# Kernel optimization log

Measured on AMD Instinct MI355X. Metric: run time of the kernel, lower is better.

## Reference

```python
import jax, jax.numpy as jnp
import numpy as np

N = 50000      # nodes
E = 800000     # edges (before self loops)
F_IN = 512     # input feature dim (num_features)
D = 128        # hidden_dim
NBLK = 3       # num_layers - 1
EPS = 1e-5


def _layernorm(x, g, b):
    mu = x.mean(-1, keepdims=True)
    var = ((x - mu) ** 2).mean(-1, keepdims=True)
    return (x - mu) / jnp.sqrt(var + EPS) * g + b


def _gatv2(x, Wl, bl, Wr, br, att, bias, src, dst, n):
    # PyG GATv2Conv, heads=1, eval mode (attention dropout off), self loops in src/dst
    xl = x @ Wl + bl                      # [N, D] messages (x_j side)
    xr = x @ Wr + br                      # [N, D] target side (x_i)
    e = jax.nn.leaky_relu(xl[src] + xr[dst], negative_slope=0.2)  # [E', D]
    score = e @ att                       # [E']
    smax = jax.ops.segment_max(score, dst, num_segments=n)
    ex = jnp.exp(score - smax[dst])
    denom = jax.ops.segment_sum(ex, dst, num_segments=n)
    alpha = ex / denom[dst]               # segment softmax over incoming edges
    out = jax.ops.segment_sum(alpha[:, None] * xl[src], dst, num_segments=n)
    return out + bias


def setup_inputs() -> dict:
    key = jax.random.key(0)
    ks = jax.random.split(key, 32)
    w = lambda k, shape: (jax.random.normal(k, shape, jnp.float32) * 0.02)
    p = {}
    p["x"] = jax.random.normal(ks[0], (N, F_IN), jnp.float32)
    p["edge_index"] = jax.random.randint(ks[1], (2, E), 0, N)
    p["emb_W"] = w(ks[2], (F_IN, D)); p["emb_b"] = jnp.zeros((D,), jnp.float32)
    p["ln1_g"] = jnp.ones((NBLK, D), jnp.float32); p["ln1_b"] = jnp.zeros((NBLK, D), jnp.float32)
    p["gat_Wl"] = w(ks[3], (NBLK, D, D)); p["gat_bl"] = jnp.zeros((NBLK, D), jnp.float32)
    p["gat_Wr"] = w(ks[4], (NBLK, D, D)); p["gat_br"] = jnp.zeros((NBLK, D), jnp.float32)
    p["gat_att"] = w(ks[5], (NBLK, D)); p["gat_bias"] = jnp.zeros((NBLK, D), jnp.float32)
    for i in range(NBLK):
        h = D * (i + 1)  # mlp_ratio = level = i+1
        p[f"mlp_w1_{i}"] = w(ks[6 + 2 * i], (D, h))
        p[f"mlp_w2_{i}"] = w(ks[7 + 2 * i], (h, D))
    p["attn_Wa"] = w(ks[12], (D, D)); p["attn_ba"] = jnp.zeros((D,), jnp.float32)
    p["attn_Wb"] = w(ks[13], (D, D)); p["attn_bb"] = jnp.zeros((D,), jnp.float32)
    p["attn_Wc"] = w(ks[14], (D, 1)); p["attn_bc"] = jnp.zeros((1,), jnp.float32)
    p["rho_W"] = w(ks[15], (D, D)); p["rho_b"] = jnp.zeros((D,), jnp.float32)
    p["cls_W"] = w(ks[16], (D, 4)); p["cls_b"] = jnp.zeros((4,), jnp.float32)
    return p


def reference(x, edge_index, emb_W, emb_b, ln1_g, ln1_b, gat_Wl, gat_bl, gat_Wr, gat_br,
              gat_att, gat_bias, mlp_w1_0, mlp_w2_0, mlp_w1_1, mlp_w2_1, mlp_w1_2, mlp_w2_2,
              attn_Wa, attn_ba, attn_Wb, attn_bb, attn_Wc, attn_bc, rho_W, rho_b, cls_W, cls_b):
    n = x.shape[0]
    sl = jnp.arange(n, dtype=edge_index.dtype)
    src = jnp.concatenate([edge_index[0], sl])  # add self loops (GATv2Conv default)
    dst = jnp.concatenate([edge_index[1], sl])
    h = jax.nn.relu(x @ emb_W + emb_b)          # embedding (dropout off)
    mlps = [(mlp_w1_0, mlp_w2_0), (mlp_w1_1, mlp_w2_1), (mlp_w1_2, mlp_w2_2)]
    for i in range(NBLK):
        hn = _layernorm(h, ln1_g[i], ln1_b[i])
        h = h + _gatv2(hn, gat_Wl[i], gat_bl[i], gat_Wr[i], gat_br[i], gat_att[i], gat_bias[i], src, dst, n)
        w1, w2 = mlps[i]
        # NOTE: original forward applies channel_mix directly on x (norm2 is unused)
        h = h + jax.nn.gelu(h @ w1, approximate=False) @ w2
    # Attn_Net_Gated pooling
    a = jnp.tanh(h @ attn_Wa + attn_ba)
    b = jax.nn.sigmoid(h @ attn_Wb + attn_bb)
    A = ((a * b) @ attn_Wc + attn_bc).T          # [1, N]
    h_path = jax.nn.softmax(A, axis=1) @ h       # [1, D]
    hr = jax.nn.relu(h_path @ rho_W + rho_b)
    logits = hr @ cls_W + cls_b                  # [1, 4]
    Y_hat = jnp.argmax(logits, axis=1, keepdims=True)
    hazards = jax.nn.sigmoid(logits)
    S = jnp.cumprod(1.0 - hazards, axis=1)
    return (hazards, S, Y_hat, logits)
```

## Files before the change

kernel.cpp:

```cpp
#include <hip/hip_runtime.h>
#include <math.h>


#define D 128
#define NBLK 3

typedef __attribute__((ext_vector_type(8))) short bf16x8;
typedef __attribute__((ext_vector_type(4))) float f32x4;

static __device__ __forceinline__ float bf2f(unsigned short u) {
    union { unsigned i; float f; } c; c.i = ((unsigned)u) << 16; return c.f;
}
static __device__ __forceinline__ unsigned short f2bf(float f) {
    union { float f; unsigned i; } c; c.f = f;
    unsigned r = c.i + 0x7fff + ((c.i >> 16) & 1);
    return (unsigned short)(r >> 16);
}

static __device__ __forceinline__ void gl16(const unsigned short* g, unsigned short* l) {
    __builtin_amdgcn_global_load_lds((const __attribute__((address_space(1))) void*)g,
                                     (__attribute__((address_space(3))) void*)l, 16, 0, 0);
}

__global__ void zero_k(int* deg, int* fill, float* red, int n) {
    int i = blockIdx.x * blockDim.x + threadIdx.x;
    if (i < n) { deg[i] = 0; fill[i] = 0; }
    if (i < 132) red[i] = 0.f;
}

__global__ void hist_k(const int* __restrict__ dst, int* __restrict__ deg, int E) {
    int e = blockIdx.x * blockDim.x + threadIdx.x;
    if (e < E) atomicAdd(&deg[dst[e]], 1);
}

__global__ __launch_bounds__(256) void blockscan_k(const int* __restrict__ deg,
                                                   int* __restrict__ rowptr,
                                                   int* __restrict__ bsum, int n) {
    __shared__ int tmp[256];
    const int tid = threadIdx.x;
    const int i = blockIdx.x * 256 + tid;
    int v = (i < n) ? deg[i] : 0;
    tmp[tid] = v;
    __syncthreads();
#pragma unroll
    for (int off = 1; off < 256; off <<= 1) {
        int t = (tid >= off) ? tmp[tid - off] : 0;
        __syncthreads();
        tmp[tid] += t;
        __syncthreads();
    }
    if (i < n) rowptr[i + 1] = tmp[tid];
    if (tid == 255) bsum[blockIdx.x] = tmp[255];
}

__global__ __launch_bounds__(256) void scansums_k(int* __restrict__ bsum, int nb) {
    __shared__ int tmp[256];
    const int tid = threadIdx.x;
    int v = (tid < nb) ? bsum[tid] : 0;
    tmp[tid] = v;
    __syncthreads();
#pragma unroll
    for (int off = 1; off < 256; off <<= 1) {
        int t = (tid >= off) ? tmp[tid - off] : 0;
        __syncthreads();
        tmp[tid] += t;
        __syncthreads();
    }
    if (tid < nb) bsum[tid] = tmp[tid];
}

__global__ __launch_bounds__(256) void addoff_k(int* __restrict__ rowptr,
                                                const int* __restrict__ bsum, int n) {
    int i = blockIdx.x * 256 + threadIdx.x;
    if (i == 0) rowptr[0] = 0;
    if (i < n && blockIdx.x > 0) rowptr[i + 1] += bsum[blockIdx.x - 1];
}

__global__ void scatter_k(const int* __restrict__ src, const int* __restrict__ dst,
                          const int* __restrict__ rowptr, int* __restrict__ fill,
                          int* __restrict__ esrc, int E) {
    int e = blockIdx.x * blockDim.x + threadIdx.x;
    if (e < E) {
        int d = dst[e];
        int pos = rowptr[d] + atomicAdd(&fill[d], 1);
        esrc[pos] = src[e];
    }
}

struct WDesc { const float* s; unsigned short* d; int K; int M; };
struct WPack { WDesc w[21]; };

__global__ __launch_bounds__(256) void wprep_k(WPack p) {
    WDesc d = p.w[blockIdx.y];
    const int nc = d.K / 32;
    const int chunks = (d.M / 16) * nc * 64;
    for (int i = blockIdx.x * 256 + threadIdx.x; i < chunks; i += gridDim.x * 256) {
        const int l = i & 63;
        const int c = (i >> 6) % nc;
        const int t = i / (64 * nc);
        const int m = t * 16 + (l & 15);
        const int kb = c * 32 + ((l >> 4) & 3) * 8;
#pragma unroll
        for (int j = 0; j < 8; ++j)
            d.d[(size_t)i * 8 + j] = f2bf(d.s[(size_t)(kb + j) * d.M + m]);
    }
}

__global__ __launch_bounds__(256) void bcat_k(const float* bl, const float* br,
                                              const float* ba, const float* bb,
                                              float* sb) {
    const int t = threadIdx.x;
    for (int i = 0; i < 3; ++i)
        sb[i * 256 + t] = (t < 128) ? bl[i * 128 + t] : br[i * 128 + t - 128];
    sb[3 * 256 + t] = (t < 128) ? ba[t] : bb[t - 128];
}

template <int NR, bool KM, int ACT, bool BIAS, bool ACC, bool LNM, bool A16,
          bool W32, bool W16>
__global__ __launch_bounds__(256) void rgemm_k(const void* __restrict__ Ap,
                                               const unsigned short* __restrict__ BTc,
                                               const float* __restrict__ bias,
                                               const float* __restrict__ lng,
                                               const float* __restrict__ lnb,
                                               float* __restrict__ C32,
                                               unsigned short* __restrict__ C16,
                                               int N, int strideA, int M) {
    __shared__ unsigned short Bls[128 * 128];
    const int tid = threadIdx.x;
    const int w = tid >> 6, l = tid & 63;
    const int q = l >> 4;
    int r = blockIdx.x * 64 + w * 16 + (l & 15);
    if (r > N - 1) r = N - 1;

    bf16x8 afr[4];
    auto loadA = [&](int koff) {
        if (A16) {
            const unsigned short* A = (const unsigned short*)Ap;
#pragma unroll
            for (int c = 0; c < 4; ++c)
                afr[c] = *(const bf16x8*)(A + (size_t)r * strideA + koff + c * 32 + q * 8);
        } else {
            const float* A = (const float*)Ap;
            float av[4][8];
#pragma unroll
            for (int c = 0; c < 4; ++c) {
                const float* ap = A + (size_t)r * strideA + koff + c * 32 + q * 8;
                const float4 v0 = *(const float4*)ap;
                const float4 v1 = *(const float4*)(ap + 4);
                av[c][0] = v0.x; av[c][1] = v0.y; av[c][2] = v0.z; av[c][3] = v0.w;
                av[c][4] = v1.x; av[c][5] = v1.y; av[c][6] = v1.z; av[c][7] = v1.w;
            }
            if (LNM) {
                float s = 0.f;
#pragma unroll
                for (int c = 0; c < 4; ++c)
#pragma unroll
                    for (int j = 0; j < 8; ++j) s += av[c][j];
                s += __shfl_xor(s, 16, 64); s += __shfl_xor(s, 32, 64);
                const float mu = s * (1.f / 128.f);
                float vv = 0.f;
#pragma unroll
                for (int c = 0; c < 4; ++c)
#pragma unroll
                    for (int j = 0; j < 8; ++j) { const float dd = av[c][j] - mu; vv += dd * dd; }
                vv += __shfl_xor(vv, 16, 64); vv += __shfl_xor(vv, 32, 64);
                const float rs = rsqrtf(vv * (1.f / 128.f) + 1e-5f);
#pragma unroll
                for (int c = 0; c < 4; ++c) {
                    const int kb = c * 32 + q * 8;
                    const float4 g0 = *(const float4*)(lng + kb);
                    const float4 g1 = *(const float4*)(lng + kb + 4);
                    const float4 b0 = *(const float4*)(lnb + kb);
                    const float4 b1 = *(const float4*)(lnb + kb + 4);
                    const float gg[8] = {g0.x, g0.y, g0.z, g0.w, g1.x, g1.y, g1.z, g1.w};
                    const float bb[8] = {b0.x, b0.y, b0.z, b0.w, b1.x, b1.y, b1.z, b1.w};
#pragma unroll
                    for (int j = 0; j < 8; ++j)
                        av[c][j] = (av[c][j] - mu) * rs * gg[j] + bb[j];
                }
            }
#pragma unroll
            for (int c = 0; c < 4; ++c)
#pragma unroll
                for (int j = 0; j < 8; ++j) afr[c][j] = (short)f2bf(av[c][j]);
        }
    };

    f32x4 acc[8];
#pragma unroll
    for (int t = 0; t < 8; ++t) acc[t] = (f32x4){0.f, 0.f, 0.f, 0.f};

    if (!KM) loadA(0);

    const int rb = blockIdx.x * 64 + w * 16 + q * 4;
    auto epi = [&](int col0) {
#pragma unroll
        for (int t = 0; t < 8; ++t) {
            const int col = col0 + t * 16 + (l & 15);
            const float bv = BIAS ? bias[col] : 0.f;
#pragma unroll
            for (int rr = 0; rr < 4; ++rr) {
                const int row = rb + rr;
                if (row >= N) continue;
                float xv = acc[t][rr] + bv;
                if (ACC) xv += C32[(size_t)row * M + col];
                if (ACT == 1) xv = fmaxf(xv, 0.f);
                else if (ACT == 2) xv = 0.5f * xv * (1.f + erff(xv * 0.70710678118654752f));
                if (W32) C32[(size_t)row * M + col] = xv;
                if (W16) C16[(size_t)row * M + col] = f2bf(xv);
            }
        }
    };

#pragma unroll
    for (int rnd = 0; rnd < NR; ++rnd) {
        if (rnd) __syncthreads();
        const unsigned short* bsrc = BTc + (size_t)rnd * 16384;
#pragma unroll
        for (int i = 0; i < 8; ++i) {
            const int idx = i * 256 + tid;
            gl16(bsrc + (size_t)idx * 8, &Bls[idx * 8]);
        }
        if (KM) loadA(rnd * 128);
        __syncthreads();
#pragma unroll
        for (int c = 0; c < 4; ++c)
#pragma unroll
            for (int t = 0; t < 8; ++t) {
                const bf16x8 bfr = *(const bf16x8*)&Bls[((t * 4 + c) * 64 + l) * 8];
                acc[t] = __builtin_amdgcn_mfma_f32_16x16x32_bf16(afr[c], bfr, acc[t], 0, 0, 0);
            }
        if (!KM) {
            epi(rnd * 128);
#pragma unroll
            for (int t = 0; t < 8; ++t) acc[t] = (f32x4){0.f, 0.f, 0.f, 0.f};
        }
    }
    if (KM) epi(0);
}

__global__ __launch_bounds__(256) void gat3_k(const unsigned short* __restrict__ X,
                                              const float* __restrict__ att,
                                              const float* __restrict__ gbias,
                                              const int* __restrict__ rowptr,
                                              const int* __restrict__ esrc,
                                              float* __restrict__ H, int n) {
    const int l = threadIdx.x & 63;
    const int node = blockIdx.x * 4 + (threadIdx.x >> 6);
    if (node >= n) return;
    const int q = l >> 4;
    const int d0 = (l & 15) * 8;

    float a8[8], xr[8], xs[8];
    {
        const float4 t0 = *(const float4*)&att[d0];
        const float4 t1 = *(const float4*)&att[d0 + 4];
        a8[0] = t0.x; a8[1] = t0.y; a8[2] = t0.z; a8[3] = t0.w;
        a8[4] = t1.x; a8[5] = t1.y; a8[6] = t1.z; a8[7] = t1.w;
        const bf16x8 uxs = *(const bf16x8*)&X[(size_t)node * 256 + d0];
        const bf16x8 uxr = *(const bf16x8*)&X[(size_t)node * 256 + 128 + d0];
#pragma unroll
        for (int j = 0; j < 8; ++j) {
            xs[j] = bf2f((unsigned short)uxs[j]);
            xr[j] = bf2f((unsigned short)uxr[j]);
        }
    }

    float sc = 0.f;
#pragma unroll
    for (int j = 0; j < 8; ++j) {
        const float e = xs[j] + xr[j];
        sc = fmaf(a8[j], fmaxf(e, 0.2f * e), sc);
    }
#pragma unroll
    for (int m = 1; m < 16; m <<= 1) sc += __shfl_xor(sc, m, 64);
    const float wself = __expf(sc);
    float dsum = (q == 0) ? wself : 0.f;
    float acc[8];
#pragma unroll
    for (int j = 0; j < 8; ++j) acc[j] = (q == 0) ? wself * xs[j] : 0.f;

    const int p1 = rowptr[node + 1];
    int p = rowptr[node] + q;
    bool v0 = p < p1, v1 = p + 4 < p1, v2 = p + 8 < p1;
    int i2 = v2 ? esrc[p + 8] : 0;
    bf16x8 u0, u1;
    if (v0) u0 = *(const bf16x8*)&X[(size_t)esrc[p] * 256 + d0];
    if (v1) u1 = *(const bf16x8*)&X[(size_t)esrc[p + 4] * 256 + d0];
    while (v0) {
        bf16x8 u2;
        if (v2) u2 = *(const bf16x8*)&X[(size_t)i2 * 256 + d0];
        const bool v3 = p + 12 < p1;
        const int i3 = v3 ? esrc[p + 12] : 0;

        float xl[8];
#pragma unroll
        for (int j = 0; j < 8; ++j) xl[j] = bf2f((unsigned short)u0[j]);
        float e_sc = 0.f;
#pragma unroll
        for (int j = 0; j < 8; ++j) {
            const float e = xl[j] + xr[j];
            e_sc = fmaf(a8[j], fmaxf(e, 0.2f * e), e_sc);
        }
#pragma unroll
        for (int m = 1; m < 16; m <<= 1) e_sc += __shfl_xor(e_sc, m, 64);
        const float wgt = __expf(e_sc);
        dsum += wgt;
#pragma unroll
        for (int j = 0; j < 8; ++j) acc[j] = fmaf(wgt, xl[j], acc[j]);

        u0 = u1; u1 = u2; i2 = i3;
        v0 = v1; v1 = v2; v2 = v3;
        p += 4;
    }

#pragma unroll
    for (int m = 16; m < 64; m <<= 1) {
        dsum += __shfl_xor(dsum, m, 64);
#pragma unroll
        for (int j = 0; j < 8; ++j) acc[j] += __shfl_xor(acc[j], m, 64);
    }

    if (q == 0) {
        const float inv = 1.f / dsum;
        const size_t o = (size_t)node * D + d0;
        float4 h0 = *(const float4*)&H[o];
        float4 h1 = *(const float4*)&H[o + 4];
        float hv[8] = {h0.x, h0.y, h0.z, h0.w, h1.x, h1.y, h1.z, h1.w};
#pragma unroll
        for (int j = 0; j < 8; ++j) hv[j] += acc[j] * inv + gbias[d0 + j];
        *(float4*)&H[o]     = make_float4(hv[0], hv[1], hv[2], hv[3]);
        *(float4*)&H[o + 4] = make_float4(hv[4], hv[5], hv[6], hv[7]);
    }
}

__global__ __launch_bounds__(256) void attnpool_k(const float* __restrict__ H,
                                                  const unsigned short* __restrict__ BTc,
                                                  const float* __restrict__ bias,
                                                  const float* __restrict__ Wc,
                                                  const float* __restrict__ bc,
                                                  float* __restrict__ red, int N) {
    __shared__ unsigned short Bls[128 * 128];
    __shared__ float sacc[4][128];
    __shared__ float sdn[4];
    const int tid = threadIdx.x;
    const int w = tid >> 6, l = tid & 63;
    const int q = l >> 4, l15 = l & 15;
    const int rowbase = blockIdx.x * 64 + w * 16;
    int r = rowbase + l15;
    if (r > N - 1) r = N - 1;

    float av[4][8];
    bf16x8 afr[4];
#pragma unroll
    for (int c = 0; c < 4; ++c) {
        const float* ap = H + (size_t)r * D + c * 32 + q * 8;
        const float4 v0 = *(const float4*)ap;
        const float4 v1 = *(const float4*)(ap + 4);
        av[c][0] = v0.x; av[c][1] = v0.y; av[c][2] = v0.z; av[c][3] = v0.w;
        av[c][4] = v1.x; av[c][5] = v1.y; av[c][6] = v1.z; av[c][7] = v1.w;
#pragma unroll
        for (int j = 0; j < 8; ++j) afr[c][j] = (short)f2bf(av[c][j]);
    }

    float th[8][4];
    f32x4 acc[8];

#pragma unroll
    for (int rnd = 0; rnd < 2; ++rnd) {
        if (rnd) __syncthreads();
        const unsigned short* bsrc = BTc + (size_t)rnd * 16384;
#pragma unroll
        for (int i = 0; i < 8; ++i) {
            const int idx = i * 256 + tid;
            gl16(bsrc + (size_t)idx * 8, &Bls[idx * 8]);
        }
#pragma unroll
        for (int t = 0; t < 8; ++t) acc[t] = (f32x4){0.f, 0.f, 0.f, 0.f};
        __syncthreads();
#pragma unroll
        for (int c = 0; c < 4; ++c)
#pragma unroll
            for (int t = 0; t < 8; ++t) {
                const bf16x8 bfr = *(const bf16x8*)&Bls[((t * 4 + c) * 64 + l) * 8];
                acc[t] = __builtin_amdgcn_mfma_f32_16x16x32_bf16(afr[c], bfr, acc[t], 0, 0, 0);
            }
        if (rnd == 0) {
#pragma unroll
            for (int t = 0; t < 8; ++t) {
                const float bv = bias[t * 16 + l15];
#pragma unroll
                for (int rr = 0; rr < 4; ++rr) th[t][rr] = tanhf(acc[t][rr] + bv);
            }
        }
    }

    float pa[4] = {0.f, 0.f, 0.f, 0.f};
#pragma unroll
    for (int t = 0; t < 8; ++t) {
        const float bv = bias[128 + t * 16 + l15];
        const float wcv = Wc[t * 16 + l15];
#pragma unroll
        for (int rr = 0; rr < 4; ++rr) {
            const float sg = 1.f / (1.f + __expf(-(acc[t][rr] + bv)));
            pa[rr] = fmaf(th[t][rr] * sg, wcv, pa[rr]);
        }
    }
#pragma unroll
    for (int m = 1; m < 16; m <<= 1)
#pragma unroll
        for (int rr = 0; rr < 4; ++rr) pa[rr] += __shfl_xor(pa[rr], m, 64);

    const float bcv = bc[0];
    float wgt[4];
#pragma unroll
    for (int rr = 0; rr < 4; ++rr) {
        const int row = blockIdx.x * 64 + w * 16 + q * 4 + rr;
        wgt[rr] = (row < N) ? __expf(pa[rr] + bcv) : 0.f;
    }
    float s = wgt[0] + wgt[1] + wgt[2] + wgt[3];
    s += __shfl_xor(s, 16, 64);
    s += __shfl_xor(s, 32, 64);
    if (l == 0) sdn[w] = s;

    const int sl = ((l15 >> 2) << 4);
    float wv[4];
#pragma unroll
    for (int rr = 0; rr < 4; ++rr) wv[rr] = __shfl(wgt[rr], sl, 64);
    const int rsel = l15 & 3;
    float wm = (rsel == 0) ? wv[0] : (rsel == 1) ? wv[1] : (rsel == 2) ? wv[2] : wv[3];

#pragma unroll
    for (int c = 0; c < 4; ++c) {
        float pv[8];
#pragma unroll
        for (int j = 0; j < 8; ++j) pv[j] = wm * av[c][j];
#pragma unroll
        for (int m = 1; m < 16; m <<= 1)
#pragma unroll
            for (int j = 0; j < 8; ++j) pv[j] += __shfl_xor(pv[j], m, 64);
        if (l15 == 0) {
#pragma unroll
            for (int j = 0; j < 8; ++j) sacc[w][c * 32 + q * 8 + j] = pv[j];
        }
    }
    __syncthreads();
    if (tid < 128) {
        const float tot = sacc[0][tid] + sacc[1][tid] + sacc[2][tid] + sacc[3][tid];
        atomicAdd(&red[tid], tot);
    }
    if (tid == 0)
        atomicAdd(&red[128], sdn[0] + sdn[1] + sdn[2] + sdn[3]);
}

__global__ __launch_bounds__(128) void final_k(const float* __restrict__ red,
                                               const float* __restrict__ rho_W,
                                               const float* __restrict__ rho_b,
                                               const float* __restrict__ cls_W,
                                               const float* __restrict__ cls_b,
                                               float* __restrict__ out) {
    __shared__ float hp[128];
    __shared__ float hr[128];
    __shared__ float lg[4];
    const int t = threadIdx.x;
    hp[t] = red[t] / red[128];
    __syncthreads();
    float s = rho_b[t];
    for (int k = 0; k < 128; ++k) s = fmaf(hp[k], rho_W[k * 128 + t], s);
    hr[t] = fmaxf(s, 0.f);
    __syncthreads();
    if (t < 4) {
        float l = cls_b[t];
        for (int k = 0; k < 128; ++k) l = fmaf(hr[k], cls_W[k * 4 + t], l);
        lg[t] = l;
    }
    __syncthreads();
    if (t == 0) {
        float hz[4], S[4];
        for (int c = 0; c < 4; ++c) hz[c] = 1.f / (1.f + expf(-lg[c]));
        S[0] = 1.f - hz[0];
        for (int c = 1; c < 4; ++c) S[c] = S[c - 1] * (1.f - hz[c]);
        int am = 0; float bm = lg[0];
        for (int c = 1; c < 4; ++c) if (lg[c] > bm) { bm = lg[c]; am = c; }
        out[0] = hz[0]; out[1] = hz[1]; out[2] = hz[2]; out[3] = hz[3];
        out[4] = S[0];  out[5] = S[1];  out[6] = S[2];  out[7] = S[3];
        out[8] = (float)am;
        out[9] = lg[0]; out[10] = lg[1]; out[11] = lg[2]; out[12] = lg[3];
    }
}

static inline int cdiv(int a, int b) { return (a + b - 1) / b; }

extern "C" void kernel_launch(void* const* d_in, const int* in_sizes, int n_in,
                              void* d_out, int out_size, void* d_ws, size_t ws_size,
                              hipStream_t stream) {
    const float* x      = (const float*)d_in[0];
    const int*   ei     = (const int*)d_in[1];
    const float* emb_W  = (const float*)d_in[2];
    const float* emb_b  = (const float*)d_in[3];
    const float* ln1_g  = (const float*)d_in[4];
    const float* ln1_b  = (const float*)d_in[5];
    const float* gat_Wl = (const float*)d_in[6];
    const float* gat_bl = (const float*)d_in[7];
    const float* gat_Wr = (const float*)d_in[8];
    const float* gat_br = (const float*)d_in[9];
    const float* gat_att  = (const float*)d_in[10];
    const float* gat_bias = (const float*)d_in[11];
    const float* mlp_w1[NBLK] = {(const float*)d_in[12], (const float*)d_in[14], (const float*)d_in[16]};
    const float* mlp_w2[NBLK] = {(const float*)d_in[13], (const float*)d_in[15], (const float*)d_in[17]};
    const float* attn_Wa = (const float*)d_in[18];
    const float* attn_ba = (const float*)d_in[19];
    const float* attn_Wb = (const float*)d_in[20];
    const float* attn_bb = (const float*)d_in[21];
    const float* attn_Wc = (const float*)d_in[22];
    const float* attn_bc = (const float*)d_in[23];
    const float* rho_W   = (const float*)d_in[24];
    const float* rho_b   = (const float*)d_in[25];
    const float* cls_W   = (const float*)d_in[26];
    const float* cls_b   = (const float*)d_in[27];
    float* out = (float*)d_out;

    const int N = in_sizes[0] / 512;
    const int E = in_sizes[1] / 2;
    const int* src = ei;
    const int* dst = ei + E;
    const int gx = cdiv(N, 64);

    char* base = (char*)d_ws;
    float* H = (float*)base;
    unsigned short* X = (unsigned short*)(H + (size_t)N * D);
    unsigned short* T = X + (size_t)N * 256;
    float* red  = (float*)(T + (size_t)N * 384);
    float* sb   = red + 132;
    unsigned short* wbuf = (unsigned short*)(sb + 1024);
    int* esrc   = (int*)(wbuf + 393216);
    int* deg    = esrc + E;
    int* rowptr = deg + N;
    int* fill   = rowptr + N + 1;
    int* bsum   = fill + N;

    unsigned short* embT = wbuf;
    unsigned short* gatT = wbuf + 4 * 16384;
    unsigned short* w1T0 = gatT + 6 * 16384;
    unsigned short* w1T1 = w1T0 + 16384;
    unsigned short* w1T2 = w1T1 + 2 * 16384;
    unsigned short* w2T0 = w1T2 + 3 * 16384;
    unsigned short* w2T1 = w2T0 + 16384;
    unsigned short* w2T2 = w2T1 + 2 * 16384;
    unsigned short* attT = w2T2 + 3 * 16384;
    unsigned short* w1T[NBLK] = {w1T0, w1T1, w1T2};
    unsigned short* w2T[NBLK] = {w2T0, w2T1, w2T2};

    const int nb = cdiv(N, 256);
    zero_k<<<cdiv(N, 256), 256, 0, stream>>>(deg, fill, red, N);
    hist_k<<<cdiv(E, 256), 256, 0, stream>>>(dst, deg, E);
    blockscan_k<<<nb, 256, 0, stream>>>(deg, rowptr, bsum, N);
    scansums_k<<<1, 256, 0, stream>>>(bsum, nb);
    addoff_k<<<nb, 256, 0, stream>>>(rowptr, bsum, N);
    scatter_k<<<cdiv(E, 256), 256, 0, stream>>>(src, dst, rowptr, fill, esrc, E);

    {
        WPack p;
        int di = 0;
        for (int r = 0; r < 4; ++r)
            p.w[di++] = {emb_W + (size_t)r * 128 * 128, embT + (size_t)r * 16384, 128, 128};
        for (int i = 0; i < 3; ++i) {
            p.w[di++] = {gat_Wl + (size_t)i * 16384, gatT + (size_t)(2 * i) * 16384, 128, 128};
            p.w[di++] = {gat_Wr + (size_t)i * 16384, gatT + (size_t)(2 * i + 1) * 16384, 128, 128};
        }
        for (int i = 0; i < 3; ++i)
            p.w[di++] = {mlp_w1[i], w1T[i], 128, 128 * (i + 1)};
        for (int i = 0; i < 3; ++i)
            for (int r = 0; r <= i; ++r)
                p.w[di++] = {mlp_w2[i] + (size_t)r * 128 * 128, w2T[i] + (size_t)r * 16384, 128, 128};
        p.w[di++] = {attn_Wa, attT, 128, 128};
        p.w[di++] = {attn_Wb, attT + 16384, 128, 128};
        wprep_k<<<dim3(32, 21), 256, 0, stream>>>(p);
    }
    bcat_k<<<1, 256, 0, stream>>>(gat_bl, gat_br, attn_ba, attn_bb, sb);

    rgemm_k<4, true, 1, true, false, false, false, true, false>
        <<<gx, 256, 0, stream>>>(x, embT, emb_b, nullptr, nullptr,
                                 H, nullptr, N, 512, 128);

    for (int i = 0; i < NBLK; ++i) {
        rgemm_k<2, false, 0, true, false, true, false, false, true>
            <<<gx, 256, 0, stream>>>(H, gatT + (size_t)(2 * i) * 16384, sb + i * 256,
                                     ln1_g + i * D, ln1_b + i * D, nullptr, X, N, 128, 256);
        gat3_k<<<cdiv(N, 4), 256, 0, stream>>>(X, gat_att + i * D, gat_bias + i * D,
                                               rowptr, esrc, H, N);
        const int h = D * (i + 1);
        if (i == 0)
            rgemm_k<1, false, 2, false, false, false, false, false, true>
                <<<gx, 256, 0, stream>>>(H, w1T[i], nullptr, nullptr, nullptr,
                                         nullptr, T, N, 128, h);
        else if (i == 1)
            rgemm_k<2, false, 2, false, false, false, false, false, true>
                <<<gx, 256, 0, stream>>>(H, w1T[i], nullptr, nullptr, nullptr,
                                         nullptr, T, N, 128, h);
        else
            rgemm_k<3, false, 2, false, false, false, false, false, true>
                <<<gx, 256, 0, stream>>>(H, w1T[i], nullptr, nullptr, nullptr,
                                         nullptr, T, N, 128, h);
        if (i == 0)
            rgemm_k<1, true, 0, false, true, false, true, true, false>
                <<<gx, 256, 0, stream>>>(T, w2T[i], nullptr, nullptr, nullptr,
                                         H, nullptr, N, h, 128);
        else if (i == 1)
            rgemm_k<2, true, 0, false, true, false, true, true, false>
                <<<gx, 256, 0, stream>>>(T, w2T[i], nullptr, nullptr, nullptr,
                                         H, nullptr, N, h, 128);
        else
            rgemm_k<3, true, 0, false, true, false, true, true, false>
                <<<gx, 256, 0, stream>>>(T, w2T[i], nullptr, nullptr, nullptr,
                                         H, nullptr, N, h, 128);
    }

    attnpool_k<<<gx, 256, 0, stream>>>(H, attT, sb + 3 * 256, attn_Wc, attn_bc, red, N);
    final_k<<<1, 128, 0, stream>>>(red, rho_W, rho_b, cls_W, cls_b, out);
}
```

Baseline: 702.1 us.

## Fuse embedding, MLP, LayerNorm and GAT projections into per-stage row kernels

Replaces the generic rgemm launches with three fused kernels. start_k does the embedding, LN and GAT projection. bridge_k does MLP w1→GELU→w2 plus residual, then LN and the next GAT projection. head_k does the last MLP plus gated attention pooling. The GELU intermediate T now stays in LDS staging instead of going through global memory, which removes the T buffer and the extra reads and writes of H. The cost is higher LDS use per block (about 66KB), which may cut occupancy, and extra barriers between the fused stages.

```diff
diff --git a/kernel.cpp b/kernel.cpp
--- a/kernel.cpp
+++ b/kernel.cpp
@@ -4,6 +4,7 @@
 
 #define D 128
 #define NBLK 3
+#define STG_STRIDE 132
 
 typedef __attribute__((ext_vector_type(8))) short bf16x8;
 typedef __attribute__((ext_vector_type(4))) float f32x4;
@@ -16,10 +17,12 @@
     unsigned r = c.i + 0x7fff + ((c.i >> 16) & 1);
     return (unsigned short)(r >> 16);
 }
-
 static __device__ __forceinline__ void gl16(const unsigned short* g, unsigned short* l) {
     __builtin_amdgcn_global_load_lds((const __attribute__((address_space(1))) void*)g,
                                      (__attribute__((address_space(3))) void*)l, 16, 0, 0);
+}
+static __device__ __forceinline__ float gelu_f(float x) {
+    return 0.5f * x * (1.f + erff(x * 0.70710678118654752f));
 }
 
 __global__ void zero_k(int* deg, int* fill, float* red, int n) {
@@ -115,128 +118,436 @@
     sb[3 * 256 + t] = (t < 128) ? ba[t] : bb[t - 128];
 }
 
-template <int NR, bool KM, int ACT, bool BIAS, bool ACC, bool LNM, bool A16,
-          bool W32, bool W16>
-__global__ __launch_bounds__(256) void rgemm_k(const void* __restrict__ Ap,
-                                               const unsigned short* __restrict__ BTc,
-                                               const float* __restrict__ bias,
+
+static __device__ __forceinline__ void stage_blob(const unsigned short* src,
+                                                  unsigned short* wls, int tid) {
+#pragma unroll
+    for (int i = 0; i < 8; ++i) {
+        const int idx = i * 256 + tid;
+        gl16(src + (size_t)idx * 8, &wls[idx * 8]);
+    }
+}
+
+static __device__ __forceinline__ void ln_row(float av[4][8], const float* lng,
+                                              const float* lnb, int q) {
+    float s = 0.f;
+#pragma unroll
+    for (int c = 0; c < 4; ++c)
+#pragma unroll
+        for (int j = 0; j < 8; ++j) s += av[c][j];
+    s += __shfl_xor(s, 16, 64); s += __shfl_xor(s, 32, 64);
+    const float mu = s * (1.f / 128.f);
+    float vv = 0.f;
+#pragma unroll
+    for (int c = 0; c < 4; ++c)
+#pragma unroll
+        for (int j = 0; j < 8; ++j) { const float dd = av[c][j] - mu; vv += dd * dd; }
+    vv += __shfl_xor(vv, 16, 64); vv += __shfl_xor(vv, 32, 64);
+    const float rs = rsqrtf(vv * (1.f / 128.f) + 1e-5f);
+#pragma unroll
+    for (int c = 0; c < 4; ++c) {
+        const int kb = c * 32 + q * 8;
+        const float4 g0 = *(const float4*)(lng + kb);
+        const float4 g1 = *(const float4*)(lng + kb + 4);
+        const float4 b0 = *(const float4*)(lnb + kb);
+        const float4 b1 = *(const float4*)(lnb + kb + 4);
+        const float gg[8] = {g0.x, g0.y, g0.z, g0.w, g1.x, g1.y, g1.z, g1.w};
+        const float bb[8] = {b0.x, b0.y, b0.z, b0.w, b1.x, b1.y, b1.z, b1.w};
+#pragma unroll
+        for (int j = 0; j < 8; ++j)
+            av[c][j] = (av[c][j] - mu) * rs * gg[j] + bb[j];
+    }
+}
+
+static __device__ __forceinline__ void gatproj(const bf16x8 xfr[4],
+                                               const unsigned short* gatc,
+                                               const float* sb256,
+                                               unsigned short* X,
+                                               unsigned short* wls,
+                                               int rowbase, int w, int l, int N,
+                                               int tid) {
+    const int q = l >> 4, l15 = l & 15;
+#pragma unroll
+    for (int rnd = 0; rnd < 2; ++rnd) {
+        __syncthreads();
+        stage_blob(gatc + (size_t)rnd * 16384, wls, tid);
+        f32x4 acc[8];
+#pragma unroll
+        for (int t = 0; t < 8; ++t) acc[t] = (f32x4){0.f, 0.f, 0.f, 0.f};
+        __syncthreads();
+#pragma unroll
+        for (int c = 0; c < 4; ++c)
+#pragma unroll
+            for (int t = 0; t < 8; ++t) {
+                const bf16x8 bfr = *(const bf16x8*)&wls[((t * 4 + c) * 64 + l) * 8];
+                acc[t] = __builtin_amdgcn_mfma_f32_16x16x32_bf16(xfr[c], bfr, acc[t], 0, 0, 0);
+            }
+#pragma unroll
+        for (int t = 0; t < 8; ++t) {
+            const int col = rnd * 128 + t * 16 + l15;
+            const float bv = sb256[col];
+#pragma unroll
+            for (int rr = 0; rr < 4; ++rr) {
+                const int row = rowbase + w * 16 + q * 4 + rr;
+                if (row < N) X[(size_t)row * 256 + col] = f2bf(acc[t][rr] + bv);
+            }
+        }
+    }
+}
+
+__global__ __launch_bounds__(256) void start_k(const float* __restrict__ x,
+                                               const unsigned short* __restrict__ embc,
+                                               const float* __restrict__ emb_b,
+                                               const unsigned short* __restrict__ gatc,
                                                const float* __restrict__ lng,
                                                const float* __restrict__ lnb,
-                                               float* __restrict__ C32,
-                                               unsigned short* __restrict__ C16,
-                                               int N, int strideA, int M) {
-    __shared__ unsigned short Bls[128 * 128];
+                                               const float* __restrict__ sb256,
+                                               float* __restrict__ H,
+                                               unsigned short* __restrict__ X, int N) {
+    __shared__ unsigned short wls[16384];
+    __shared__ float stg[64 * STG_STRIDE];
     const int tid = threadIdx.x;
-    const int w = tid >> 6, l = tid & 63;
-    const int q = l >> 4;
-    int r = blockIdx.x * 64 + w * 16 + (l & 15);
+    const int w = tid >> 6, l = tid & 63, q = l >> 4, l15 = l & 15;
+    const int rowbase = blockIdx.x * 64;
+    int r = rowbase + w * 16 + l15;
+    const bool rv = r < N; if (!rv) r = N - 1;
+
+    f32x4 accH[8];
+#pragma unroll
+    for (int t = 0; t < 8; ++t) accH[t] = (f32x4){0.f, 0.f, 0.f, 0.f};
+
+#pragma unroll
+    for (int rnd = 0; rnd < 4; ++rnd) {
+        if (rnd) __syncthreads();
+        stage_blob(embc + (size_t)rnd * 16384, wls, tid);
+        bf16x8 afr[4];
+#pragma unroll
+        for (int c = 0; c < 4; ++c) {
+            const float* ap = x + (size_t)r * 512 + rnd * 128 + c * 32 + q * 8;
+            const float4 v0 = *(const float4*)ap;
+            const float4 v1 = *(const float4*)(ap + 4);
+            afr[c][0] = (short)f2bf(v0.x); afr[c][1] = (short)f2bf(v0.y);
+            afr[c][2] = (short)f2bf(v0.z); afr[c][3] = (short)f2bf(v0.w);
+            afr[c][4] = (short)f2bf(v1.x); afr[c][5] = (short)f2bf(v1.y);
+            afr[c][6] = (short)f2bf(v1.z); afr[c][7] = (short)f2bf(v1.w);
+        }
+        __syncthreads();
+#pragma unroll
+        for (int c = 0; c < 4; ++c)
+#pragma unroll
+            for (int t = 0; t < 8; ++t) {
+                const bf16x8 bfr = *(const bf16x8*)&wls[((t * 4 + c) * 64 + l) * 8];
+                accH[t] = __builtin_amdgcn_mfma_f32_16x16x32_bf16(afr[c], bfr, accH[t], 0, 0, 0);
+            }
+    }
+
+    __syncthreads();
+#pragma unroll
+    for (int t = 0; t < 8; ++t) {
+        const int col = t * 16 + l15;
+        const float bv = emb_b[col];
+#pragma unroll
+        for (int rr = 0; rr < 4; ++rr) {
+            const int row = rowbase + w * 16 + q * 4 + rr;
+            const float hv = fmaxf(accH[t][rr] + bv, 0.f);
+            if (row < N) H[(size_t)row * D + col] = hv;
+            stg[(w * 16 + q * 4 + rr) * STG_STRIDE + col] = hv;
+        }
+    }
+    __syncthreads();
+
+    float av[4][8];
+#pragma unroll
+    for (int c = 0; c < 4; ++c)
+#pragma unroll
+        for (int j = 0; j < 8; ++j)
+            av[c][j] = stg[(w * 16 + l15) * STG_STRIDE + c * 32 + q * 8 + j];
+    ln_row(av, lng, lnb, q);
+    bf16x8 xfr[4];
+#pragma unroll
+    for (int c = 0; c < 4; ++c)
+#pragma unroll
+        for (int j = 0; j < 8; ++j) xfr[c][j] = (short)f2bf(av[c][j]);
+
+    gatproj(xfr, gatc, sb256, X, wls, rowbase, w, l, N, tid);
+}
+
+template <int NMR>
+__global__ __launch_bounds__(256) void bridge_k(float* __restrict__ H,
+                                                const unsigned short* __restrict__ w1c,
+                                                const unsigned short* __restrict__ w2c,
+                                                const unsigned short* __restrict__ gatc,
+                                                const float* __restrict__ lng,
+                                                const float* __restrict__ lnb,
+                                                const float* __restrict__ sb256,
+                                                unsigned short* __restrict__ X, int N) {
+    __shared__ unsigned short wls[16384];
+    __shared__ float stg[64 * STG_STRIDE];
+    const int tid = threadIdx.x;
+    const int w = tid >> 6, l = tid & 63, q = l >> 4, l15 = l & 15;
+    const int rowbase = blockIdx.x * 64;
+    int r = rowbase + w * 16 + l15;
+    const bool rv = r < N; if (!rv) r = N - 1;
+
+    float av[4][8];
+    bf16x8 afr[4];
+#pragma unroll
+    for (int c = 0; c < 4; ++c) {
+        const float* ap = H + (size_t)r * D + c * 32 + q * 8;
+        const float4 v0 = *(const float4*)ap;
+        const float4 v1 = *(const float4*)(ap + 4);
+        av[c][0] = v0.x; av[c][1] = v0.y; av[c][2] = v0.z; av[c][3] = v0.w;
+        av[c][4] = v1.x; av[c][5] = v1.y; av[c][6] = v1.z; av[c][7] = v1.w;
+#pragma unroll
+        for (int j = 0; j < 8; ++j) afr[c][j] = (short)f2bf(av[c][j]);
+    }
+
+    f32x4 accH[8];
+#pragma unroll
+    for (int t = 0; t < 8; ++t) accH[t] = (f32x4){0.f, 0.f, 0.f, 0.f};
+
+#pragma unroll
+    for (int rnd = 0; rnd < NMR; ++rnd) {
+        __syncthreads();
+        stage_blob(w1c + (size_t)rnd * 16384, wls, tid);
+        f32x4 accT[8];
+#pragma unroll
+        for (int t = 0; t < 8; ++t) accT[t] = (f32x4){0.f, 0.f, 0.f, 0.f};
+        __syncthreads();
+#pragma unroll
+        for (int c = 0; c < 4; ++c)
+#pragma unroll
+            for (int t = 0; t < 8; ++t) {
+                const bf16x8 bfr = *(const bf16x8*)&wls[((t * 4 + c) * 64 + l) * 8];
+                accT[t] = __builtin_amdgcn_mfma_f32_16x16x32_bf16(afr[c], bfr, accT[t], 0, 0, 0);
+            }
+        __syncthreads();
+#pragma unroll
+        for (int t = 0; t < 8; ++t)
+#pragma unroll
+            for (int rr = 0; rr < 4; ++rr)
+                stg[(w * 16 + q * 4 + rr) * STG_STRIDE + t * 16 + l15] = gelu_f(accT[t][rr]);
+        stage_blob(w2c + (size_t)rnd * 16384, wls, tid);
+        __syncthreads();
+        bf16x8 tfr[4];
+#pragma unroll
+        for (int c = 0; c < 4; ++c)
+#pragma unroll
+            for (int j = 0; j < 8; ++j)
+                tfr[c][j] = (short)f2bf(stg[(w * 16 + l15) * STG_STRIDE + c * 32 + q * 8 + j]);
+#pragma unroll
+        for (int c = 0; c < 4; ++c)
+#pragma unroll
+            for (int t = 0; t < 8; ++t) {
+                const bf16x8 bfr = *(const bf16x8*)&wls[((t * 4 + c) * 64 + l) * 8];
+                accH[t] = __builtin_amdgcn_mfma_f32_16x16x32_bf16(tfr[c], bfr, accH[t], 0, 0, 0);
+            }
+    }
+
+    __syncthreads();
+#pragma unroll
+    for (int t = 0; t < 8; ++t)
+#pragma unroll
+        for (int rr = 0; rr < 4; ++rr)
+            stg[(w * 16 + q * 4 + rr) * STG_STRIDE + t * 16 + l15] = accH[t][rr];
+    __syncthreads();
+#pragma unroll
+    for (int c = 0; c < 4; ++c)
+#pragma unroll
+        for (int j = 0; j < 8; ++j)
+            av[c][j] += stg[(w * 16 + l15) * STG_STRIDE + c * 32 + q * 8 + j];
+
+    if (rv) {
+#pragma unroll
+        for (int c = 0; c < 4; ++c) {
+            float* hp = H + (size_t)r * D + c * 32 + q * 8;
+            *(float4*)hp       = make_float4(av[c][0], av[c][1], av[c][2], av[c][3]);
+            *(float4*)(hp + 4) = make_float4(av[c][4], av[c][5], av[c][6], av[c][7]);
+        }
+    }
+
+    ln_row(av, lng, lnb, q);
+    bf16x8 xfr[4];
+#pragma unroll
+    for (int c = 0; c < 4; ++c)
+#pragma unroll
+        for (int j = 0; j < 8; ++j) xfr[c][j] = (short)f2bf(av[c][j]);
+
+    gatproj(xfr, gatc, sb256, X, wls, rowbase, w, l, N, tid);
+}
+
+__global__ __launch_bounds__(256) void head_k(const float* __restrict__ H,
+                                              const unsigned short* __restrict__ w1c,
+                                              const unsigned short* __restrict__ w2c,
+                                              const unsigned short* __restrict__ attc,
+                                              const float* __restrict__ sb256,
+                                              const float* __restrict__ Wc,
+                                              const float* __restrict__ bc,
+                                              float* __restrict__ red, int N) {
+    __shared__ unsigned short wls[16384];
+    __shared__ float stg[64 * STG_STRIDE];
+    __shared__ float sacc[4][128];
+    __shared__ float sdn[4];
+    const int tid = threadIdx.x;
+    const int w = tid >> 6, l = tid & 63, q = l >> 4, l15 = l & 15;
+    const int rowbase = blockIdx.x * 64;
+    int r = rowbase + w * 16 + l15;
     if (r > N - 1) r = N - 1;
 
+    float av[4][8];
     bf16x8 afr[4];
-    auto loadA = [&](int koff) {
-        if (A16) {
-            const unsigned short* A = (const unsigned short*)Ap;
-#pragma unroll
-            for (int c = 0; c < 4; ++c)
-                afr[c] = *(const bf16x8*)(A + (size_t)r * strideA + koff + c * 32 + q * 8);
-        } else {
-            const float* A = (const float*)Ap;
-            float av[4][8];
-#pragma unroll
-            for (int c = 0; c < 4; ++c) {
-                const float* ap = A + (size_t)r * strideA + koff + c * 32 + q * 8;
-                const float4 v0 = *(const float4*)ap;
-                const float4 v1 = *(const float4*)(ap + 4);
-                av[c][0] = v0.x; av[c][1] = v0.y; av[c][2] = v0.z; av[c][3] = v0.w;
-                av[c][4] = v1.x; av[c][5] = v1.y; av[c][6] = v1.z; av[c][7] = v1.w;
-            }
-            if (LNM) {
-                float s = 0.f;
-#pragma unroll
-                for (int c = 0; c < 4; ++c)
-#pragma unroll
-                    for (int j = 0; j < 8; ++j) s += av[c][j];
-                s += __shfl_xor(s, 16, 64); s += __shfl_xor(s, 32, 64);
-                const float mu = s * (1.f / 128.f);
-                float vv = 0.f;
-#pragma unroll
-                for (int c = 0; c < 4; ++c)
-#pragma unroll
-                    for (int j = 0; j < 8; ++j) { const float dd = av[c][j] - mu; vv += dd * dd; }
-                vv += __shfl_xor(vv, 16, 64); vv += __shfl_xor(vv, 32, 64);
-                const float rs = rsqrtf(vv * (1.f / 128.f) + 1e-5f);
-#pragma unroll
-                for (int c = 0; c < 4; ++c) {
-                    const int kb = c * 32 + q * 8;
-                    const float4 g0 = *(const float4*)(lng + kb);
-                    const float4 g1 = *(const float4*)(lng + kb + 4);
-                    const float4 b0 = *(const float4*)(lnb + kb);
-                    const float4 b1 = *(const float4*)(lnb + kb + 4);
-                    const float gg[8] = {g0.x, g0.y, g0.z, g0.w, g1.x, g1.y, g1.z, g1.w};
-                    const float bb[8] = {b0.x, b0.y, b0.z, b0.w, b1.x, b1.y, b1.z, b1.w};
-#pragma unroll
-                    for (int j = 0; j < 8; ++j)
-                        av[c][j] = (av[c][j] - mu) * rs * gg[j] + bb[j];
-                }
-            }
-#pragma unroll
-            for (int c = 0; c < 4; ++c)
-#pragma unroll
-                for (int j = 0; j < 8; ++j) afr[c][j] = (short)f2bf(av[c][j]);
-        }
-    };
-
+#pragma unroll
+    for (int c = 0; c < 4; ++c) {
+        const float* ap = H + (size_t)r * D + c * 32 + q * 8;
+        const float4 v0 = *(const float4*)ap;
+        const float4 v1 = *(const float4*)(ap + 4);
+        av[c][0] = v0.x; av[c][1] = v0.y; av[c][2] = v0.z; av[c][3] = v0.w;
+        av[c][4] = v1.x; av[c][5] = v1.y; av[c][6] = v1.z; av[c][7] = v1.w;
+#pragma unroll
+        for (int j = 0; j < 8; ++j) afr[c][j] = (short)f2bf(av[c][j]);
+    }
+
+    f32x4 accH[8];
+#pragma unroll
+    for (int t = 0; t < 8; ++t) accH[t] = (f32x4){0.f, 0.f, 0.f, 0.f};
+
+#pragma unroll
+    for (int rnd = 0; rnd < 3; ++rnd) {
+        __syncthreads();
+        stage_blob(w1c + (size_t)rnd * 16384, wls, tid);
+        f32x4 accT[8];
+#pragma unroll
+        for (int t = 0; t < 8; ++t) accT[t] = (f32x4){0.f, 0.f, 0.f, 0.f};
+        __syncthreads();
+#pragma unroll
+        for (int c = 0; c < 4; ++c)
+#pragma unroll
+            for (int t = 0; t < 8; ++t) {
+                const bf16x8 bfr = *(const bf16x8*)&wls[((t * 4 + c) * 64 + l) * 8];
+                accT[t] = __builtin_amdgcn_mfma_f32_16x16x32_bf16(afr[c], bfr, accT[t], 0, 0, 0);
+            }
+        __syncthreads();
+#pragma unroll
+        for (int t = 0; t < 8; ++t)
+#pragma unroll
+            for (int rr = 0; rr < 4; ++rr)
+                stg[(w * 16 + q * 4 + rr) * STG_STRIDE + t * 16 + l15] = gelu_f(accT[t][rr]);
+        stage_blob(w2c + (size_t)rnd * 16384, wls, tid);
+        __syncthreads();
+        bf16x8 tfr[4];
+#pragma unroll
+        for (int c = 0; c < 4; ++c)
+#pragma unroll
+            for (int j = 0; j < 8; ++j)
+                tfr[c][j] = (short)f2bf(stg[(w * 16 + l15) * STG_STRIDE + c * 32 + q * 8 + j]);
+#pragma unroll
+        for (int c = 0; c < 4; ++c)
+#pragma unroll
+            for (int t = 0; t < 8; ++t) {
+                const bf16x8 bfr = *(const bf16x8*)&wls[((t * 4 + c) * 64 + l) * 8];
+                accH[t] = __builtin_amdgcn_mfma_f32_16x16x32_bf16(tfr[c], bfr, accH[t], 0, 0, 0);
+            }
+    }
+
+    __syncthreads();
+#pragma unroll
+    for (int t = 0; t < 8; ++t)
+#pragma unroll
+        for (int rr = 0; rr < 4; ++rr)
+            stg[(w * 16 + q * 4 + rr) * STG_STRIDE + t * 16 + l15] = accH[t][rr];
+    __syncthreads();
+#pragma unroll
+    for (int c = 0; c < 4; ++c)
+#pragma unroll
+        for (int j = 0; j < 8; ++j)
+            av[c][j] += stg[(w * 16 + l15) * STG_STRIDE + c * 32 + q * 8 + j];
+#pragma unroll
+    for (int c = 0; c < 4; ++c)
+#pragma unroll
+        for (int j = 0; j < 8; ++j) afr[c][j] = (short)f2bf(av[c][j]);
+
+    float th[8][4];
     f32x4 acc[8];
 #pragma unroll
-    for (int t = 0; t < 8; ++t) acc[t] = (f32x4){0.f, 0.f, 0.f, 0.f};
-
-    if (!KM) loadA(0);
-
-    const int rb = blockIdx.x * 64 + w * 16 + q * 4;
-    auto epi = [&](int col0) {
-#pragma unroll
-        for (int t = 0; t < 8; ++t) {
-            const int col = col0 + t * 16 + (l & 15);
-            const float bv = BIAS ? bias[col] : 0.f;
-#pragma unroll
-            for (int rr = 0; rr < 4; ++rr) {
-                const int row = rb + rr;
-                if (row >= N) continue;
-                float xv = acc[t][rr] + bv;
-                if (ACC) xv += C32[(size_t)row * M + col];
-                if (ACT == 1) xv = fmaxf(xv, 0.f);
-                else if (ACT == 2) xv = 0.5f * xv * (1.f + erff(xv * 0.70710678118654752f));
-                if (W32) C32[(size_t)row * M + col] = xv;
-                if (W16) C16[(size_t)row * M + col] = f2bf(xv);
-            }
-        }
-    };
-
-#pragma unroll
-    for (int rnd = 0; rnd < NR; ++rnd) {
-        if (rnd) __syncthreads();
-        const unsigned short* bsrc = BTc + (size_t)rnd * 16384;
-#pragma unroll
-        for (int i = 0; i < 8; ++i) {
-            const int idx = i * 256 + tid;
-            gl16(bsrc + (size_t)idx * 8, &Bls[idx * 8]);
-        }
-        if (KM) loadA(rnd * 128);
+    for (int rnd = 0; rnd < 2; ++rnd) {
+        __syncthreads();
+        stage_blob(attc + (size_t)rnd * 16384, wls, tid);
+#pragma unroll
+        for (int t = 0; t < 8; ++t) acc[t] = (f32x4){0.f, 0.f, 0.f, 0.f};
         __syncthreads();
 #pragma unroll
         for (int c = 0; c < 4; ++c)
 #pragma unroll
             for (int t = 0; t < 8; ++t) {
-                const bf16x8 bfr = *(const bf16x8*)&Bls[((t * 4 + c) * 64 + l) * 8];
+                const bf16x8 bfr = *(const bf16x8*)&wls[((t * 4 + c) * 64 + l) * 8];
                 acc[t] = __builtin_amdgcn_mfma_f32_16x16x32_bf16(afr[c], bfr, acc[t], 0, 0, 0);
             }
-        if (!KM) {
-            epi(rnd * 128);
-#pragma unroll
-            for (int t = 0; t < 8; ++t) acc[t] = (f32x4){0.f, 0.f, 0.f, 0.f};
-        }
-    }
-    if (KM) epi(0);
+        if (rnd == 0) {
+#pragma unroll
+            for (int t = 0; t < 8; ++t) {
+                const float bv = sb256[t * 16 + l15];
+#pragma unroll
+                for (int rr = 0; rr < 4; ++rr) th[t][rr] = tanhf(acc[t][rr] + bv);
+            }
+        }
+    }
+
+    float pa[4] = {0.f, 0.f, 0.f, 0.f};
+#pragma unroll
+    for (int t = 0; t < 8; ++t) {
+        const float bv = sb256[128 + t * 16 + l15];
+        const float wcv = Wc[t * 16 + l15];
+#pragma unroll
+        for (int rr = 0; rr < 4; ++rr) {
+            const float sg = 1.f / (1.f + __expf(-(acc[t][rr] + bv)));
+            pa[rr] = fmaf(th[t][rr] * sg, wcv, pa[rr]);
+        }
+    }
+#pragma unroll
+    for (int m = 1; m < 16; m <<= 1)
+#pragma unroll
+        for (int rr = 0; rr < 4; ++rr) pa[rr] += __shfl_xor(pa[rr], m, 64);
+
+    const float bcv = bc[0];
+    float wgt[4];
+#pragma unroll
+    for (int rr = 0; rr < 4; ++rr) {
+        const int row = rowbase + w * 16 + q * 4 + rr;
+        wgt[rr] = (row < N) ? __expf(pa[rr] + bcv) : 0.f;
+    }
+    float s = wgt[0] + wgt[1] + wgt[2] + wgt[3];
+    s += __shfl_xor(s, 16, 64);
+    s += __shfl_xor(s, 32, 64);
+    if (l == 0) sdn[w] = s;
+
+    const int sl = ((l15 >> 2) << 4);
+    float wv[4];
+#pragma unroll
+    for (int rr = 0; rr < 4; ++rr) wv[rr] = __shfl(wgt[rr], sl, 64);
+    const int rsel = l15 & 3;
+    const float wm = (rsel == 0) ? wv[0] : (rsel == 1) ? wv[1] : (rsel == 2) ? wv[2] : wv[3];
+
+#pragma unroll
+    for (int c = 0; c < 4; ++c) {
+        float pv[8];
+#pragma unroll
+        for (int j = 0; j < 8; ++j) pv[j] = wm * av[c][j];
+#pragma unroll
+        for (int m = 1; m < 16; m <<= 1)
+#pragma unroll
+            for (int j = 0; j < 8; ++j) pv[j] += __shfl_xor(pv[j], m, 64);
+        if (l15 == 0) {
+#pragma unroll
+            for (int j = 0; j < 8; ++j) sacc[w][c * 32 + q * 8 + j] = pv[j];
+        }
+    }
+    __syncthreads();
+    if (tid < 128) {
+        const float tot = sacc[0][tid] + sacc[1][tid] + sacc[2][tid] + sacc[3][tid];
+        atomicAdd(&red[tid], tot);
+    }
+    if (tid == 0)
+        atomicAdd(&red[128], sdn[0] + sdn[1] + sdn[2] + sdn[3]);
 }
 
 __global__ __launch_bounds__(256) void gat3_k(const unsigned short* __restrict__ X,
@@ -332,125 +643,6 @@
         *(float4*)&H[o]     = make_float4(hv[0], hv[1], hv[2], hv[3]);
         *(float4*)&H[o + 4] = make_float4(hv[4], hv[5], hv[6], hv[7]);
     }
-}
-
-__global__ __launch_bounds__(256) void attnpool_k(const float* __restrict__ H,
-                                                  const unsigned short* __restrict__ BTc,
-                                                  const float* __restrict__ bias,
-                                                  const float* __restrict__ Wc,
-                                                  const float* __restrict__ bc,
-                                                  float* __restrict__ red, int N) {
-    __shared__ unsigned short Bls[128 * 128];
-    __shared__ float sacc[4][128];
-    __shared__ float sdn[4];
-    const int tid = threadIdx.x;
-    const int w = tid >> 6, l = tid & 63;
-    const int q = l >> 4, l15 = l & 15;
-    const int rowbase = blockIdx.x * 64 + w * 16;
-    int r = rowbase + l15;
-    if (r > N - 1) r = N - 1;
-
-    float av[4][8];
-    bf16x8 afr[4];
-#pragma unroll
-    for (int c = 0; c < 4; ++c) {
-        const float* ap = H + (size_t)r * D + c * 32 + q * 8;
-        const float4 v0 = *(const float4*)ap;
-        const float4 v1 = *(const float4*)(ap + 4);
-        av[c][0] = v0.x; av[c][1] = v0.y; av[c][2] = v0.z; av[c][3] = v0.w;
-        av[c][4] = v1.x; av[c][5] = v1.y; av[c][6] = v1.z; av[c][7] = v1.w;
-#pragma unroll
-        for (int j = 0; j < 8; ++j) afr[c][j] = (short)f2bf(av[c][j]);
-    }
-
-    float th[8][4];
-    f32x4 acc[8];
-
-#pragma unroll
-    for (int rnd = 0; rnd < 2; ++rnd) {
-        if (rnd) __syncthreads();
-        const unsigned short* bsrc = BTc + (size_t)rnd * 16384;
-#pragma unroll
-        for (int i = 0; i < 8; ++i) {
-            const int idx = i * 256 + tid;
-            gl16(bsrc + (size_t)idx * 8, &Bls[idx * 8]);
-        }
-#pragma unroll
-        for (int t = 0; t < 8; ++t) acc[t] = (f32x4){0.f, 0.f, 0.f, 0.f};
-        __syncthreads();
-#pragma unroll
-        for (int c = 0; c < 4; ++c)
-#pragma unroll
-            for (int t = 0; t < 8; ++t) {
-                const bf16x8 bfr = *(const bf16x8*)&Bls[((t * 4 + c) * 64 + l) * 8];
-                acc[t] = __builtin_amdgcn_mfma_f32_16x16x32_bf16(afr[c], bfr, acc[t], 0, 0, 0);
-            }
-        if (rnd == 0) {
-#pragma unroll
-            for (int t = 0; t < 8; ++t) {
-                const float bv = bias[t * 16 + l15];
-#pragma unroll
-                for (int rr = 0; rr < 4; ++rr) th[t][rr] = tanhf(acc[t][rr] + bv);
-            }
-        }
-    }
-
-    float pa[4] = {0.f, 0.f, 0.f, 0.f};
-#pragma unroll
-    for (int t = 0; t < 8; ++t) {
-        const float bv = bias[128 + t * 16 + l15];
-        const float wcv = Wc[t * 16 + l15];
-#pragma unroll
-        for (int rr = 0; rr < 4; ++rr) {
-            const float sg = 1.f / (1.f + __expf(-(acc[t][rr] + bv)));
-            pa[rr] = fmaf(th[t][rr] * sg, wcv, pa[rr]);
-        }
-    }
-#pragma unroll
-    for (int m = 1; m < 16; m <<= 1)
-#pragma unroll
-        for (int rr = 0; rr < 4; ++rr) pa[rr] += __shfl_xor(pa[rr], m, 64);
-
-    const float bcv = bc[0];
-    float wgt[4];
-#pragma unroll
-    for (int rr = 0; rr < 4; ++rr) {
-        const int row = blockIdx.x * 64 + w * 16 + q * 4 + rr;
-        wgt[rr] = (row < N) ? __expf(pa[rr] + bcv) : 0.f;
-    }
-    float s = wgt[0] + wgt[1] + wgt[2] + wgt[3];
-    s += __shfl_xor(s, 16, 64);
-    s += __shfl_xor(s, 32, 64);
-    if (l == 0) sdn[w] = s;
-
-    const int sl = ((l15 >> 2) << 4);
-    float wv[4];
-#pragma unroll
-    for (int rr = 0; rr < 4; ++rr) wv[rr] = __shfl(wgt[rr], sl, 64);
-    const int rsel = l15 & 3;
-    float wm = (rsel == 0) ? wv[0] : (rsel == 1) ? wv[1] : (rsel == 2) ? wv[2] : wv[3];
-
-#pragma unroll
-    for (int c = 0; c < 4; ++c) {
-        float pv[8];
-#pragma unroll
-        for (int j = 0; j < 8; ++j) pv[j] = wm * av[c][j];
-#pragma unroll
-        for (int m = 1; m < 16; m <<= 1)
-#pragma unroll
-            for (int j = 0; j < 8; ++j) pv[j] += __shfl_xor(pv[j], m, 64);
-        if (l15 == 0) {
-#pragma unroll
-            for (int j = 0; j < 8; ++j) sacc[w][c * 32 + q * 8 + j] = pv[j];
-        }
-    }
-    __syncthreads();
-    if (tid < 128) {
-        const float tot = sacc[0][tid] + sacc[1][tid] + sacc[2][tid] + sacc[3][tid];
-        atomicAdd(&red[tid], tot);
-    }
-    if (tid == 0)
-        atomicAdd(&red[128], sdn[0] + sdn[1] + sdn[2] + sdn[3]);
 }
 
 __global__ __launch_bounds__(128) void final_k(const float* __restrict__ red,
@@ -529,8 +721,7 @@
     char* base = (char*)d_ws;
     float* H = (float*)base;
     unsigned short* X = (unsigned short*)(H + (size_t)N * D);
-    unsigned short* T = X + (size_t)N * 256;
-    float* red  = (float*)(T + (size_t)N * 384);
+    float* red  = (float*)(X + (size_t)N * 256);
     float* sb   = red + 132;
     unsigned short* wbuf = (unsigned short*)(sb + 1024);
     int* esrc   = (int*)(wbuf + 393216);
@@ -579,43 +770,18 @@
     }
     bcat_k<<<1, 256, 0, stream>>>(gat_bl, gat_br, attn_ba, attn_bb, sb);
 
-    rgemm_k<4, true, 1, true, false, false, false, true, false>
-        <<<gx, 256, 0, stream>>>(x, embT, emb_b, nullptr, nullptr,
-                                 H, nullptr, N, 512, 128);
-
-    for (int i = 0; i < NBLK; ++i) {
-        rgemm_k<2, false, 0, true, false, true, false, false, true>
-            <<<gx, 256, 0, stream>>>(H, gatT + (size_t)(2 * i) * 16384, sb + i * 256,
-                                     ln1_g + i * D, ln1_b + i * D, nullptr, X, N, 128, 256);
-        gat3_k<<<cdiv(N, 4), 256, 0, stream>>>(X, gat_att + i * D, gat_bias + i * D,
-                                               rowptr, esrc, H, N);
-        const int h = D * (i + 1);
-        if (i == 0)
-            rgemm_k<1, false, 2, false, false, false, false, false, true>
-                <<<gx, 256, 0, stream>>>(H, w1T[i], nullptr, nullptr, nullptr,
-                                         nullptr, T, N, 128, h);
-        else if (i == 1)
-            rgemm_k<2, false, 2, false, false, false, false, false, true>
-                <<<gx, 256, 0, stream>>>(H, w1T[i], nullptr, nullptr, nullptr,
-                                         nullptr, T, N, 128, h);
-        else
-            rgemm_k<3, false, 2, false, false, false, false, false, true>
-                <<<gx, 256, 0, stream>>>(H, w1T[i], nullptr, nullptr, nullptr,
-                                         nullptr, T, N, 128, h);
-        if (i == 0)
-            rgemm_k<1, true, 0, false, true, false, true, true, false>
-                <<<gx, 256, 0, stream>>>(T, w2T[i], nullptr, nullptr, nullptr,
-                                         H, nullptr, N, h, 128);
-        else if (i == 1)
-            rgemm_k<2, true, 0, false, true, false, true, true, false>
-                <<<gx, 256, 0, stream>>>(T, w2T[i], nullptr, nullptr, nullptr,
-                                         H, nullptr, N, h, 128);
-        else
-            rgemm_k<3, true, 0, false, true, false, true, true, false>
-                <<<gx, 256, 0, stream>>>(T, w2T[i], nullptr, nullptr, nullptr,
-                                         H, nullptr, N, h, 128);
-    }
-
-    attnpool_k<<<gx, 256, 0, stream>>>(H, attT, sb + 3 * 256, attn_Wc, attn_bc, red, N);
+    start_k<<<gx, 256, 0, stream>>>(x, embT, emb_b, gatT, ln1_g, ln1_b, sb, H, X, N);
+    gat3_k<<<cdiv(N, 4), 256, 0, stream>>>(X, gat_att, gat_bias, rowptr, esrc, H, N);
+
+    bridge_k<1><<<gx, 256, 0, stream>>>(H, w1T[0], w2T[0], gatT + 2 * 16384,
+                                        ln1_g + D, ln1_b + D, sb + 256, X, N);
+    gat3_k<<<cdiv(N, 4), 256, 0, stream>>>(X, gat_att + D, gat_bias + D, rowptr, esrc, H, N);
+
+    bridge_k<2><<<gx, 256, 0, stream>>>(H, w1T[1], w2T[1], gatT + 4 * 16384,
+                                        ln1_g + 2 * D, ln1_b + 2 * D, sb + 512, X, N);
+    gat3_k<<<cdiv(N, 4), 256, 0, stream>>>(X, gat_att + 2 * D, gat_bias + 2 * D, rowptr, esrc, H, N);
+
+    head_k<<<gx, 256, 0, stream>>>(H, w1T[2], w2T[2], attT, sb + 3 * 256,
+                                   attn_Wc, attn_bc, red, N);
     final_k<<<1, 128, 0, stream>>>(red, rho_W, rho_b, cls_W, cls_b, out);
 }
```

Result: faster. 657.3 us (-6.4%).
